# Performance work log

Measured on AMD Instinct MI355X. Metric: run time of the kernel, lower is better.

Reference implementation:

```python
import jax, jax.numpy as jnp
import numpy as np
import math

LMAX = 8
NUM_VECTORS = 64
N_COEF = (LMAX + 1) * (LMAX + 2) // 2  # 45 even-order SH coefficients


def _dfact(n):
    out = 1.0
    k = n
    while k > 1:
        out *= k
        k -= 2
    return out


def sh_tournier_all(xyz, lmax=LMAX):
    """Real even-order spherical harmonics, orders 0,2,...,lmax concatenated
    (m = -l..l within each order), with the Tournier (-1)^|m| sign applied and
    the input permuted xyz -> yzx and normalized (as in the torch module).
    Output: xyz.shape[:-1] + (45,). Fully polynomial in the unit vector, so it
    is smooth/differentiable (no atan2 / division by sin(theta))."""
    yzx = xyz[..., jnp.array([1, 2, 0])]
    r = jnp.sqrt(jnp.sum(yzx * yzx, axis=-1, keepdims=True) + 1e-12)
    u = yzx / r
    px, py, pz = u[..., 0], u[..., 1], u[..., 2]
    # A_m = rho^m cos(m*phi), B_m = rho^m sin(m*phi) via Chebyshev-style recurrence
    A = [jnp.ones_like(px)]
    Bv = [jnp.zeros_like(px)]
    for m in range(1, lmax + 1):
        A.append(px * A[-1] - py * Bv[-1])
        Bv.append(px * Bv[-1] + py * A[-2])
    # Q[l,m] = P_l^m / sin^m(theta): polynomial in pz (Condon-Shortley included)
    Q = {}
    for m in range(lmax + 1):
        qmm = ((-1.0) ** m) * _dfact(2 * m - 1)
        Q[(m, m)] = jnp.full_like(pz, qmm)
        if m < lmax:
            Q[(m + 1, m)] = (2 * m + 1) * qmm * pz
        for l in range(m + 2, lmax + 1):
            Q[(l, m)] = ((2 * l - 1) * pz * Q[(l - 1, m)]
                         - (l + m - 1) * Q[(l - 2, m)]) / (l - m)
    blocks = []
    sqrt2 = math.sqrt(2.0)
    for l in range(0, lmax + 1, 2):
        comps = []
        for m in range(-l, l + 1):
            am = abs(m)
            K = math.sqrt((2 * l + 1) / (4 * math.pi)
                          * math.factorial(l - am) / math.factorial(l + am))
            sgn = -1.0 if am % 2 == 1 else 1.0  # Tournier normalization sign
            if m < 0:
                val = sqrt2 * K * Q[(l, am)] * Bv[am]
            elif m == 0:
                val = K * Q[(l, 0)]
            else:
                val = sqrt2 * K * Q[(l, am)] * A[am]
            comps.append(sgn * val)
        blocks.append(jnp.stack(comps, axis=-1))
    return jnp.concatenate(blocks, axis=-1)


def _forward(image, affine, psf_vectors, M_p):
    B, X, Y, Z, C = image.shape
    V = psf_vectors.shape[0]
    img = jnp.transpose(image.reshape(B, -1, C), (0, 2, 1))      # [B,C,N]
    affine_inv = jnp.linalg.inv(affine)                           # [B,X,Y,Z,3,3]
    w = jnp.einsum('vc,bcn->bvn', M_p, img)                       # PSF weights [B,V,N]
    vi = psf_vectors.T                                            # [3,V]
    vi_hat = affine_inv @ vi                                      # [B,X,Y,Z,3,V]
    M_prime = sh_tournier_all(jnp.swapaxes(vi_hat, -1, -2))       # [B,X,Y,Z,V,C]
    # modulation: |A^{-1} v| / det(A^{-1}) per voxel per vector
    mod = (jnp.sqrt(jnp.sum(vi_hat * vi_hat, axis=-2))
           / jnp.linalg.det(affine_inv)[..., None])               # [B,X,Y,Z,V]
    mod = jnp.moveaxis(mod, -1, 1).reshape(B, V, -1)              # [B,V,N]
    w_mod = mod * w                                               # [B,V,N]
    # per-voxel small GEMV: out[b,n,c] = sum_v M_prime[b,n,v,c] * w_mod[b,v,n]
    out = jnp.einsum('bnvc,bvn->bnc', M_prime.reshape(B, -1, V, C), w_mod)
    return out.reshape(image.shape)


def setup_inputs() -> dict:
    key = jax.random.key(0)
    k1, k2, k3 = jax.random.split(key, 3)
    B, X, Y, Z = 1, 32, 32, 32
    image = jax.random.normal(k1, (B, X, Y, Z, N_COEF), dtype=jnp.float32)
    # per-voxel Jacobian field: near-identity so inverse/det are well-conditioned
    affine = (jnp.eye(3, dtype=jnp.float32)
              + 0.1 * jax.random.normal(k2, (B, X, Y, Z, 3, 3), dtype=jnp.float32))
    psf = jax.random.normal(k3, (NUM_VECTORS, 3), dtype=jnp.float32)
    psf = psf / jnp.linalg.norm(psf, axis=-1, keepdims=True)      # unit PSF directions
    M0 = sh_tournier_all(psf)                                     # [V,45]
    M_p = jnp.linalg.pinv(M0.T)                                   # pinv([45,V]) -> [V,45]
    return {"image": image, "affine": affine, "psf_vectors": psf, "M_p": M_p}


def reference(image, affine, psf_vectors, M_p):
    return _forward(image, affine, psf_vectors, M_p)
```

## Files before the change

### kernel.cpp

```cpp
#include <hip/hip_runtime.h>
#include <type_traits>
#include <utility>

#define CDIM   45
#define LMAXX  8
#define WAVES_PB 4
#define VOXPB  64
#define VDIM   64
#define VPT    (VDIM / WAVES_PB)

constexpr double PI_D = 3.14159265358979323846;

constexpr double dfactd(int n){ double o=1.0; for(int k=n;k>1;k-=2) o*=k; return o; }
constexpr double factd (int n){ double o=1.0; for(int k=2;k<=n;++k) o*=k; return o; }
constexpr double csqrtd(double x){
  if(x<=0.0) return 0.0;
  double g = x>1.0 ? x : 1.0;
  for(int i=0;i<200;++i) g = 0.5*(g + x/g);
  return g;
}

constexpr double CPf(int m, int l){
  double K = csqrtd((2.0*l+1.0)/(4.0*PI_D)*factd(l-m)/factd(l+m));
  if (m==0) return K;
  return ((m&1)?-1.0:1.0)*csqrtd(2.0)*K;
}

struct SHTab {
  float c1[LMAXX+1][LMAXX+1];
  float c2[LMAXX+1][LMAXX+1];
  float qmm[LMAXX+1];
  float qnx[LMAXX+1];
};

constexpr SHTab makeTab(){
  SHTab t{};
  for(int m=0;m<=LMAXX;++m){
    double q = ((m&1)?-1.0:1.0)*dfactd(2*m-1);
    t.qmm[m]=(float)(q*CPf(m,m));
    t.qnx[m]=(m<LMAXX)?(float)((2.0*m+1.0)*q*CPf(m,m+1)):0.0f;
    for(int l=m+2;l<=LMAXX;++l){
      t.c1[m][l]=(float)((2.0*l-1.0)/(double)(l-m)*CPf(m,l)/CPf(m,l-1));
      t.c2[m][l]=(float)((double)(l+m-1)/(double)(l-m)*CPf(m,l)/CPf(m,l-2));
    }
  }
  return t;
}
constexpr SHTab SHT = makeTab();

constexpr int offL(int l){ return l==0?0 : (l==2?1 : (l==4?6 : (l==6?15 : 28))); }

template<int N, typename F>
__device__ __forceinline__ void cunroll(F&& f){
  if constexpr (N > 0){
    cunroll<N-1>(f);
    f(std::integral_constant<int, N-1>{});
  }
}

__global__ __launch_bounds__(256, 3)
void fodf_reorient_kernel(const float* __restrict__ image,
                          const float* __restrict__ affine,
                          const float* __restrict__ psf,
                          const float* __restrict__ Mp,
                          float* __restrict__ out,
                          int Nvox)
{
  __shared__ float red[WAVES_PB][VOXPB][CDIM+3];

  const int tid  = threadIdx.x;
  const int lane = tid & 63;
  const int wvi  = __builtin_amdgcn_readfirstlane(tid >> 6);
  const int voxBase = blockIdx.x * VOXPB;
  const int vox  = voxBase + lane;
  const bool valid = vox < Nvox;

  float img[CDIM];
  if (valid){
    const float* ip = image + (long long)vox * CDIM;
    #pragma unroll
    for(int c=0;c<CDIM;++c) img[c] = ip[c];
  } else {
    #pragma unroll
    for(int c=0;c<CDIM;++c) img[c] = 0.0f;
  }

  float a[9];
  if (valid){
    const float* ap = affine + (long long)vox * 9;
    #pragma unroll
    for(int i=0;i<9;++i) a[i] = ap[i];
  } else {
    #pragma unroll
    for(int i=0;i<9;++i) a[i] = (i%4==0) ? 1.0f : 0.0f;
  }

  const float det = a[0]*(a[4]*a[8]-a[5]*a[7])
                  - a[1]*(a[3]*a[8]-a[5]*a[6])
                  + a[2]*(a[3]*a[7]-a[4]*a[6]);
  const float rdet = 1.0f/det;
  const float i00 =  (a[4]*a[8]-a[5]*a[7])*rdet;
  const float i01 = -(a[1]*a[8]-a[2]*a[7])*rdet;
  const float i02 =  (a[1]*a[5]-a[2]*a[4])*rdet;
  const float i10 = -(a[3]*a[8]-a[5]*a[6])*rdet;
  const float i11 =  (a[0]*a[8]-a[2]*a[6])*rdet;
  const float i12 = -(a[0]*a[5]-a[2]*a[3])*rdet;
  const float i20 =  (a[3]*a[7]-a[4]*a[6])*rdet;
  const float i21 = -(a[0]*a[7]-a[1]*a[6])*rdet;
  const float i22 =  (a[0]*a[4]-a[1]*a[3])*rdet;

  float acc[CDIM];
  #pragma unroll
  for(int c=0;c<CDIM;++c) acc[c]=0.0f;

  const int vbase = wvi * VPT;
  #pragma unroll 4
  for(int k=0;k<VPT;++k){
    const int v = vbase + k;
    const float sxv = psf[3*v+0];
    const float syv = psf[3*v+1];
    const float szv = psf[3*v+2];

    const float hx = fmaf(i00,sxv, fmaf(i01,syv, i02*szv));
    const float hy = fmaf(i10,sxv, fmaf(i11,syv, i12*szv));
    const float hz = fmaf(i20,sxv, fmaf(i21,syv, i22*szv));

    const float r2  = fmaf(hx,hx, fmaf(hy,hy, hz*hz));
    const float rin = rsqrtf(r2 + 1e-12f);
    const float px = hy*rin;
    const float py = hz*rin;
    const float pz = hx*rin;

    const float modv = r2 * rin * det;

    const float* Mrow = Mp + v*CDIM;
    float w0=0.f,w1=0.f,w2=0.f,w3=0.f;
    #pragma unroll
    for(int c=0;c<44;c+=4){
      w0 = fmaf(Mrow[c+0], img[c+0], w0);
      w1 = fmaf(Mrow[c+1], img[c+1], w1);
      w2 = fmaf(Mrow[c+2], img[c+2], w2);
      w3 = fmaf(Mrow[c+3], img[c+3], w3);
    }
    w0 = fmaf(Mrow[44], img[44], w0);
    const float wval = (w0+w1)+(w2+w3);
    const float wmod = modv * wval;

    float Aa[LMAXX+1], Bb[LMAXX+1];
    Aa[0]=wmod; Bb[0]=0.0f;
    cunroll<LMAXX>([&](auto Mc){
      constexpr int M = decltype(Mc)::value + 1;
      Aa[M] = fmaf(px, Aa[M-1], -(py*Bb[M-1]));
      Bb[M] = fmaf(px, Bb[M-1],  (py*Aa[M-1]));
    });

    cunroll<LMAXX+1>([&](auto AMc){
      constexpr int AM = decltype(AMc)::value;
      const float fa = Aa[AM];
      const float fb = Bb[AM];
      float qp2 = SHT.qmm[AM];
      float qp1 = SHT.qnx[AM]*pz;

      if constexpr ((AM&1)==0){
        if constexpr (AM==0){
          acc[0] = fmaf(qp2, fa, acc[0]);
        } else {
          acc[offL(AM)+2*AM] = fmaf(qp2, fa, acc[offL(AM)+2*AM]);
          acc[offL(AM)+0   ] = fmaf(qp2, fb, acc[offL(AM)+0   ]);
        }
      }
      if constexpr (AM<LMAXX && (((AM+1)&1)==0)){
        constexpr int L = AM+1;
        acc[offL(L)+L+AM] = fmaf(qp1, fa, acc[offL(L)+L+AM]);
        acc[offL(L)+L-AM] = fmaf(qp1, fb, acc[offL(L)+L-AM]);
      }

      constexpr int CNT = (LMAXX-AM-1) > 0 ? (LMAXX-AM-1) : 0;
      cunroll<CNT>([&](auto Lc){
        constexpr int L = AM + 2 + decltype(Lc)::value;
        constexpr float C1 = SHT.c1[AM][L];
        constexpr float C2 = SHT.c2[AM][L];
        const float q = fmaf(C1*pz, qp1, -(C2*qp2));
        qp2 = qp1; qp1 = q;
        if constexpr ((L&1)==0){
          if constexpr (AM==0){
            acc[offL(L)+L] = fmaf(q, fa, acc[offL(L)+L]);
          } else {
            acc[offL(L)+L+AM] = fmaf(q, fa, acc[offL(L)+L+AM]);
            acc[offL(L)+L-AM] = fmaf(q, fb, acc[offL(L)+L-AM]);
          }
        }
      });
    });
  }

  #pragma unroll
  for(int c=0;c<CDIM;++c) red[wvi][lane][c] = acc[c];
  __syncthreads();

  const int total = VOXPB * CDIM;
  for(int i = tid; i < total; i += 256){
    const int vx = i / CDIM;
    if (voxBase + vx < Nvox){
      const int c = i - vx*CDIM;
      const float s = red[0][vx][c] + red[1][vx][c]
                    + red[2][vx][c] + red[3][vx][c];
      out[(long long)voxBase*CDIM + i] = s;
    }
  }
}

extern "C" void kernel_launch(void* const* d_in, const int* in_sizes, int n_in,
                              void* d_out, int out_size, void* d_ws, size_t ws_size,
                              hipStream_t stream)
{
  const float* image  = (const float*)d_in[0];
  const float* affine = (const float*)d_in[1];
  const float* psf    = (const float*)d_in[2];
  const float* Mp     = (const float*)d_in[3];
  float* out = (float*)d_out;

  const int Nvox = in_sizes[0] / CDIM;
  const int blocks = (Nvox + VOXPB - 1) / VOXPB;

  hipLaunchKernelGGL(fodf_reorient_kernel, dim3(blocks), dim3(256), 0, stream,
                     image, affine, psf, Mp, out, Nvox);
}
```

Measured before the change: 79.47 us.

## Stage image/affine through LDS and split GEMV from SH accumulation loop

Image and affine tiles are copied into shared memory with coalesced block-wide loads, then each lane reads its own voxel from LDS. The work is also split into two loops: all 16 per-vector GEMV dot products are computed first into a small array, then the SH accumulation loop runs. The split lets the 45-element image registers die before the 45 accumulators go live, which lowers register pressure. In exchange, shared memory per block grows by about 14 KB. That may cut the number of resident blocks below the launch-bounds target. The wv[k] array is also indexed inside a non-unrolled loop, which could force it into scratch memory.

```diff
diff --git a/kernel.cpp b/kernel.cpp
--- a/kernel.cpp
+++ b/kernel.cpp
@@ -66,6 +66,8 @@
                           float* __restrict__ out,
                           int Nvox)
 {
+  __shared__ float simg[VOXPB*CDIM];
+  __shared__ float saff[VOXPB*9];
   __shared__ float red[WAVES_PB][VOXPB][CDIM+3];
 
   const int tid  = threadIdx.x;
@@ -75,25 +77,24 @@
   const int vox  = voxBase + lane;
   const bool valid = vox < Nvox;
 
+  {
+    const float* gi = image + (size_t)voxBase * CDIM;
+    const int limi = min(VOXPB*CDIM, (Nvox - voxBase)*CDIM);
+    #pragma unroll 1
+    for (int f = tid; f < limi; f += 256) simg[f] = gi[f];
+    const float* ga = affine + (size_t)voxBase * 9;
+    const int lima = min(VOXPB*9, (Nvox - voxBase)*9);
+    #pragma unroll 1
+    for (int f = tid; f < lima; f += 256) saff[f] = ga[f];
+  }
+  __syncthreads();
+
   float img[CDIM];
-  if (valid){
-    const float* ip = image + (long long)vox * CDIM;
-    #pragma unroll
-    for(int c=0;c<CDIM;++c) img[c] = ip[c];
-  } else {
-    #pragma unroll
-    for(int c=0;c<CDIM;++c) img[c] = 0.0f;
-  }
-
+  #pragma unroll
+  for(int c=0;c<CDIM;++c) img[c] = simg[lane*CDIM + c];
   float a[9];
-  if (valid){
-    const float* ap = affine + (long long)vox * 9;
-    #pragma unroll
-    for(int i=0;i<9;++i) a[i] = ap[i];
-  } else {
-    #pragma unroll
-    for(int i=0;i<9;++i) a[i] = (i%4==0) ? 1.0f : 0.0f;
-  }
+  #pragma unroll
+  for(int i=0;i<9;++i) a[i] = saff[lane*9 + i];
 
   const float det = a[0]*(a[4]*a[8]-a[5]*a[7])
                   - a[1]*(a[3]*a[8]-a[5]*a[6])
@@ -109,31 +110,12 @@
   const float i21 = -(a[0]*a[7]-a[1]*a[6])*rdet;
   const float i22 =  (a[0]*a[4]-a[1]*a[3])*rdet;
 
-  float acc[CDIM];
-  #pragma unroll
-  for(int c=0;c<CDIM;++c) acc[c]=0.0f;
-
   const int vbase = wvi * VPT;
-  #pragma unroll 4
+
+  float wv[VPT];
+  #pragma unroll 2
   for(int k=0;k<VPT;++k){
-    const int v = vbase + k;
-    const float sxv = psf[3*v+0];
-    const float syv = psf[3*v+1];
-    const float szv = psf[3*v+2];
-
-    const float hx = fmaf(i00,sxv, fmaf(i01,syv, i02*szv));
-    const float hy = fmaf(i10,sxv, fmaf(i11,syv, i12*szv));
-    const float hz = fmaf(i20,sxv, fmaf(i21,syv, i22*szv));
-
-    const float r2  = fmaf(hx,hx, fmaf(hy,hy, hz*hz));
-    const float rin = rsqrtf(r2 + 1e-12f);
-    const float px = hy*rin;
-    const float py = hz*rin;
-    const float pz = hx*rin;
-
-    const float modv = r2 * rin * det;
-
-    const float* Mrow = Mp + v*CDIM;
+    const float* Mrow = Mp + (vbase+k)*CDIM;
     float w0=0.f,w1=0.f,w2=0.f,w3=0.f;
     #pragma unroll
     for(int c=0;c<44;c+=4){
@@ -143,8 +125,31 @@
       w3 = fmaf(Mrow[c+3], img[c+3], w3);
     }
     w0 = fmaf(Mrow[44], img[44], w0);
-    const float wval = (w0+w1)+(w2+w3);
-    const float wmod = modv * wval;
+    wv[k] = (w0+w1)+(w2+w3);
+  }
+
+  float acc[CDIM];
+  #pragma unroll
+  for(int c=0;c<CDIM;++c) acc[c]=0.0f;
+
+  #pragma unroll 1
+  for(int k=0;k<VPT;++k){
+    const int v = vbase + k;
+    const float sxv = psf[3*v+0];
+    const float syv = psf[3*v+1];
+    const float szv = psf[3*v+2];
+
+    const float hx = fmaf(i00,sxv, fmaf(i01,syv, i02*szv));
+    const float hy = fmaf(i10,sxv, fmaf(i11,syv, i12*szv));
+    const float hz = fmaf(i20,sxv, fmaf(i21,syv, i22*szv));
+
+    const float r2  = fmaf(hx,hx, fmaf(hy,hy, hz*hz));
+    const float rin = rsqrtf(r2 + 1e-12f);
+    const float px = hy*rin;
+    const float py = hz*rin;
+    const float pz = hx*rin;
+
+    const float wmod = r2 * rin * det * wv[k];
 
     float Aa[LMAXX+1], Bb[LMAXX+1];
     Aa[0]=wmod; Bb[0]=0.0f;
```

After: 84.35 us. 1.06x slower.

## Split PSF-vector reduction across two blocks per tile with combine kernel

Applied to the files above, without the earlier changes.

Each voxel tile is now handled by two blocks, each covering half of the 64 PSF vectors and writing partial sums to workspace. A second kernel adds the two partials with float4 loads and writes the output. This doubles the grid (512 → 1024 blocks) to fill the CUs better on a small problem. The cost is a second launch, workspace traffic, and each voxel's image and affine being loaded twice.

```diff
diff --git a/kernel.cpp b/kernel.cpp
--- a/kernel.cpp
+++ b/kernel.cpp
@@ -7,7 +7,9 @@
 #define WAVES_PB 4
 #define VOXPB  64
 #define VDIM   64
-#define VPT    (VDIM / WAVES_PB)
+#define NSPLIT 2
+#define VPT    (VDIM / NSPLIT / WAVES_PB)
+#define TILEF  (VOXPB * CDIM)
 
 constexpr double PI_D = 3.14159265358979323846;
 
@@ -59,19 +61,22 @@
 }
 
 __global__ __launch_bounds__(256, 3)
-void fodf_reorient_kernel(const float* __restrict__ image,
-                          const float* __restrict__ affine,
-                          const float* __restrict__ psf,
-                          const float* __restrict__ Mp,
-                          float* __restrict__ out,
-                          int Nvox)
+void fodf_main(const float* __restrict__ image,
+               const float* __restrict__ affine,
+               const float* __restrict__ psf,
+               const float* __restrict__ Mp,
+               float* __restrict__ ws,
+               int Nvox)
 {
   __shared__ float red[WAVES_PB][VOXPB][CDIM+3];
 
   const int tid  = threadIdx.x;
   const int lane = tid & 63;
   const int wvi  = __builtin_amdgcn_readfirstlane(tid >> 6);
-  const int voxBase = blockIdx.x * VOXPB;
+  const int bx   = blockIdx.x;
+  const int tileIdx = bx >> 1;
+  const int half    = bx & 1;
+  const int voxBase = tileIdx * VOXPB;
   const int vox  = voxBase + lane;
   const bool valid = vox < Nvox;
 
@@ -113,7 +118,7 @@
   #pragma unroll
   for(int c=0;c<CDIM;++c) acc[c]=0.0f;
 
-  const int vbase = wvi * VPT;
+  const int vbase = half*(VDIM/NSPLIT) + wvi * VPT;
   #pragma unroll 4
   for(int k=0;k<VPT;++k){
     const int v = vbase + k;
@@ -198,14 +203,36 @@
   for(int c=0;c<CDIM;++c) red[wvi][lane][c] = acc[c];
   __syncthreads();
 
-  const int total = VOXPB * CDIM;
-  for(int i = tid; i < total; i += 256){
+  float* wp = ws + (size_t)bx * TILEF;
+  for(int i = tid; i < TILEF; i += 256){
     const int vx = i / CDIM;
-    if (voxBase + vx < Nvox){
-      const int c = i - vx*CDIM;
-      const float s = red[0][vx][c] + red[1][vx][c]
-                    + red[2][vx][c] + red[3][vx][c];
-      out[(long long)voxBase*CDIM + i] = s;
+    const int c  = i - vx*CDIM;
+    wp[i] = red[0][vx][c] + red[1][vx][c] + red[2][vx][c] + red[3][vx][c];
+  }
+}
+
+__global__ __launch_bounds__(256)
+void fodf_combine(const float* __restrict__ ws,
+                  float* __restrict__ out,
+                  int total)
+{
+  const int n4 = total >> 2;
+  const int i4 = blockIdx.x * 256 + threadIdx.x;
+  const float4* ws4 = (const float4*)ws;
+  float4* out4 = (float4*)out;
+  constexpr int T4 = TILEF / 4;
+  if (i4 < n4){
+    const int t = i4 / T4;
+    const int j = i4 - t * T4;
+    const float4 a = ws4[(size_t)(2*t  )*T4 + j];
+    const float4 b = ws4[(size_t)(2*t+1)*T4 + j];
+    out4[i4] = make_float4(a.x+b.x, a.y+b.y, a.z+b.z, a.w+b.w);
+  }
+  if (i4 == 0){
+    for (int r = n4*4; r < total; ++r){
+      const int t = r / TILEF;
+      const int j = r - t*TILEF;
+      out[r] = ws[(size_t)(2*t)*TILEF + j] + ws[(size_t)(2*t+1)*TILEF + j];
     }
   }
 }
@@ -219,10 +246,15 @@
   const float* psf    = (const float*)d_in[2];
   const float* Mp     = (const float*)d_in[3];
   float* out = (float*)d_out;
-
-  const int Nvox = in_sizes[0] / CDIM;
-  const int blocks = (Nvox + VOXPB - 1) / VOXPB;
-
-  hipLaunchKernelGGL(fodf_reorient_kernel, dim3(blocks), dim3(256), 0, stream,
-                     image, affine, psf, Mp, out, Nvox);
-}
+  float* ws  = (float*)d_ws;
+
+  const int Nvox   = in_sizes[0] / CDIM;
+  const int ntiles = (Nvox + VOXPB - 1) / VOXPB;
+  const int total  = Nvox * CDIM;
+  const int n4     = total >> 2;
+
+  hipLaunchKernelGGL(fodf_main, dim3(ntiles * NSPLIT), dim3(256), 0, stream,
+                     image, affine, psf, Mp, ws, Nvox);
+  hipLaunchKernelGGL(fodf_combine, dim3((n4 + 255)/256), dim3(256), 0, stream,
+                     ws, out, total);
+}
```

New measurement: 88.74 us. 1.12x slower.
